# Kernel tuning notes

Hardware: AMD Instinct MI355X
Metric: run time of the kernel (lower is better)

## Reference

```python
import jax, jax.numpy as jnp
import numpy as np

DIM = 2048
NUM_HEADS = 16
HEAD_DIM = DIM // NUM_HEADS
ROPE_BASE = 10000.0


def _rope_cos_sin(seq_len, head_dim, dtype):
    # lucidrains-style interleaved rotary embedding
    inv_freq = 1.0 / (ROPE_BASE ** (jnp.arange(0, head_dim, 2, dtype=jnp.float32) / head_dim))
    t = jnp.arange(seq_len, dtype=jnp.float32)
    freqs = t[:, None] * inv_freq[None, :]            # [n, d/2]
    freqs = jnp.repeat(freqs, 2, axis=-1)             # [n, d] interleaved repeat
    return jnp.cos(freqs).astype(dtype), jnp.sin(freqs).astype(dtype)


def _rotate_half(x):
    # interleaved pairs: (x1, x2) -> (-x2, x1)
    x = x.reshape(x.shape[:-1] + (x.shape[-1] // 2, 2))
    x1, x2 = x[..., 0], x[..., 1]
    return jnp.stack((-x2, x1), axis=-1).reshape(x.shape[:-2] + (-1,))


def _apply_rope(x, cos, sin):
    # x: [b, h, n, d]; cos/sin: [n, d]
    return x * cos + _rotate_half(x) * sin


def setup_inputs() -> dict:
    key = jax.random.key(0)
    ks = jax.random.split(key, 9)
    s = 1.0 / np.sqrt(DIM)
    x = jax.random.normal(ks[0], (2, 2048, DIM), dtype=jnp.float32)
    Wq = jax.random.normal(ks[1], (DIM, DIM), dtype=jnp.float32) * s
    Wk = jax.random.normal(ks[2], (DIM, DIM), dtype=jnp.float32) * s
    Wv = jax.random.normal(ks[3], (DIM, DIM), dtype=jnp.float32) * s
    Wo = jax.random.normal(ks[4], (DIM, DIM), dtype=jnp.float32) * s
    bq = jax.random.normal(ks[5], (DIM,), dtype=jnp.float32) * 0.01
    bk = jax.random.normal(ks[6], (DIM,), dtype=jnp.float32) * 0.01
    bv = jax.random.normal(ks[7], (DIM,), dtype=jnp.float32) * 0.01
    bo = jax.random.normal(ks[8], (DIM,), dtype=jnp.float32) * 0.01
    return {"x": x, "Wq": Wq, "bq": bq, "Wk": Wk, "bk": bk,
            "Wv": Wv, "bv": bv, "Wo": Wo, "bo": bo}


def reference(x, Wq, bq, Wk, bk, Wv, bv, Wo, bo):
    b, n, _ = x.shape
    h, d = NUM_HEADS, HEAD_DIM
    # Q/K/V projections; weights stored as [in, out]
    q = (x @ Wq + bq).reshape(b, n, h, d).transpose(0, 2, 1, 3)  # [b,h,n,d]
    k = (x @ Wk + bk).reshape(b, n, h, d).transpose(0, 2, 1, 3)
    v = (x @ Wv + bv).reshape(b, n, h, d).transpose(0, 2, 1, 3)
    cos, sin = _rope_cos_sin(n, d, x.dtype)
    q = _apply_rope(q, cos, sin)
    k = _apply_rope(k, cos, sin)
    # module divides q by sqrt(d), then SDPA applies its own 1/sqrt(d)
    scale = 1.0 / jnp.sqrt(jnp.asarray(d, dtype=x.dtype))
    q = q * scale
    logits = jnp.einsum('bhqd,bhkd->bhqk', q, k) * scale
    attn = jax.nn.softmax(logits, axis=-1)
    out = jnp.einsum('bhqk,bhkd->bhqd', attn, v)          # [b,h,n,d]
    out = out.transpose(0, 2, 1, 3).reshape(b, n, h * d)  # [b,n,dim]
    return out @ Wo + bo
```

## Files before the change

kernel.cpp:

```cpp
#include <hip/hip_runtime.h>
#include <hip/hip_bf16.h>
#include <math.h>

typedef unsigned short u16;
typedef unsigned int u32;
typedef __attribute__((ext_vector_type(8))) short short8;
typedef __attribute__((ext_vector_type(4))) float f32x4;

typedef const __attribute__((address_space(1))) u32 gu32;
typedef __attribute__((address_space(3))) u32 lu32;

#define DIM 2048
#define SEQ 2048
#define BATCH 2
#define NH 16
#define HD 128
#define MTOT 4096

static __device__ __forceinline__ u16 f2b(float f) {
  __hip_bfloat16 h = __float2bfloat16(f);
  return __builtin_bit_cast(u16, h);
}
static __device__ __forceinline__ float b2f(u16 u) {
  __hip_bfloat16 h = __builtin_bit_cast(__hip_bfloat16, u);
  return __bfloat162float(h);
}

static __device__ __forceinline__ void g2l16(const u16* g, u16* l) {
  __builtin_amdgcn_global_load_lds((gu32*)g, (lu32*)l, 16, 0, 0);
}

__global__ __launch_bounds__(256) void conv_x_kernel(const float* __restrict__ x,
                                                     u16* __restrict__ xb) {
  size_t i = ((size_t)blockIdx.x * 256 + threadIdx.x) * 8;
  float4 a = *(const float4*)(x + i);
  float4 b = *(const float4*)(x + i + 4);
  uint4 o;
  o.x = (u32)f2b(a.x) | ((u32)f2b(a.y) << 16);
  o.y = (u32)f2b(a.z) | ((u32)f2b(a.w) << 16);
  o.z = (u32)f2b(b.x) | ((u32)f2b(b.y) << 16);
  o.w = (u32)f2b(b.z) | ((u32)f2b(b.w) << 16);
  *(uint4*)(xb + i) = o;
}

__global__ __launch_bounds__(256) void transw_kernel(const float* __restrict__ W0,
                                                     const float* __restrict__ W1,
                                                     const float* __restrict__ W2,
                                                     const float* __restrict__ W3,
                                                     u16* __restrict__ WT) {
  __shared__ float tile[64][65];
  const float* W = (blockIdx.z == 0) ? W0 : (blockIdx.z == 1) ? W1
                 : (blockIdx.z == 2) ? W2 : W3;
  u16* dst = WT + (size_t)blockIdx.z * DIM * DIM;
  int t = threadIdx.x;
  int k0 = blockIdx.y * 64, n0 = blockIdx.x * 64;
  int c = (t & 15) * 4;
  int r = t >> 4;
#pragma unroll
  for (int i = 0; i < 4; ++i) {
    float4 v = *(const float4*)(W + (size_t)(k0 + r + 16 * i) * DIM + n0 + c);
    tile[r + 16 * i][c + 0] = v.x;
    tile[r + 16 * i][c + 1] = v.y;
    tile[r + 16 * i][c + 2] = v.z;
    tile[r + 16 * i][c + 3] = v.w;
  }
  __syncthreads();
#pragma unroll
  for (int i = 0; i < 4; ++i) {
    int rn = r + 16 * i;
    uint2 o;
    o.x = (u32)f2b(tile[c + 0][rn]) | ((u32)f2b(tile[c + 1][rn]) << 16);
    o.y = (u32)f2b(tile[c + 2][rn]) | ((u32)f2b(tile[c + 3][rn]) << 16);
    *(uint2*)(dst + (size_t)(n0 + rn) * DIM + k0 + c) = o;
  }
}

__global__ __launch_bounds__(256) void rope_table_kernel(float* __restrict__ tab) {
  int idx = blockIdx.x * 256 + threadIdx.x;
  int n = idx >> 6, j = idx & 63;
  double ang = (double)n * pow(10000.0, -(double)j / 64.0);
  tab[2 * idx + 0] = (float)cos(ang);
  tab[2 * idx + 1] = (float)sin(ang);
}

__global__ __launch_bounds__(256) void rope_kernel(u16* __restrict__ Q,
                                                   u16* __restrict__ Kt,
                                                   const float* __restrict__ tab) {
  int idx = blockIdx.x * 256 + threadIdx.x;
  int which = idx >> 22;
  int rem = idx & ((1 << 22) - 1);
  int bh = rem >> 17;
  int r2 = rem & ((1 << 17) - 1);
  int n = r2 >> 6, j = r2 & 63;
  u16* p = (which ? Kt : Q) + ((size_t)bh * SEQ + n) * HD + 2 * j;
  float c = tab[2 * (n * 64 + j) + 0], s = tab[2 * (n * 64 + j) + 1];
  u32 v = *(const u32*)p;
  float x1 = b2f((u16)(v & 0xffff)), x2 = b2f((u16)(v >> 16));
  float sc = which ? 1.0f : (1.0f / 128.0f);
  float o1 = (x1 * c - x2 * s) * sc;
  float o2 = (x2 * c + x1 * s) * sc;
  *(u32*)p = (u32)f2b(o1) | ((u32)f2b(o2) << 16);
}

__global__ __launch_bounds__(256) void gemm_kernel(const u16* __restrict__ A,
                                                   const u16* __restrict__ Bt,
                                                   const float* __restrict__ bias,
                                                   void* __restrict__ Cout, int mode) {
  __shared__ u16 Asub[128 * 64];
  __shared__ u16 Bsub[128 * 64];
  int t = threadIdx.x;
  int lane = t & 63, wid = t >> 6;
  int L15 = lane & 15, quad = lane >> 4;
  int wm = (wid >> 1) * 64, wn = (wid & 1) * 64;
  int m0 = blockIdx.y * 128, n0 = blockIdx.x * 128;
  int srow = lane >> 3;
  int schunk = lane & 7;

  f32x4 acc[4][4];
#pragma unroll
  for (int mi = 0; mi < 4; ++mi)
#pragma unroll
    for (int ni = 0; ni < 4; ++ni)
#pragma unroll
      for (int r = 0; r < 4; ++r) acc[mi][ni][r] = 0.f;

  for (int k0 = 0; k0 < DIM; k0 += 64) {
#pragma unroll
    for (int i = 0; i < 4; ++i) {
      int ra = wid * 32 + i * 8 + srow;
      int cs = schunk ^ (ra & 7);
      g2l16(A + (size_t)(m0 + ra) * DIM + k0 + cs * 8,
            Asub + (size_t)(wid * 32 + i * 8) * 64);
      g2l16(Bt + (size_t)(n0 + ra) * DIM + k0 + cs * 8,
            Bsub + (size_t)(wid * 32 + i * 8) * 64);
    }
    __syncthreads();
#pragma unroll
    for (int kc = 0; kc < 2; ++kc) {
      short8 af[4], bfr[4];
#pragma unroll
      for (int mi = 0; mi < 4; ++mi) {
        int row = wm + mi * 16 + L15;
        af[mi] = *(const short8*)(Asub + row * 64 + (((kc * 4 + quad) ^ (L15 & 7)) * 8));
      }
#pragma unroll
      for (int ni = 0; ni < 4; ++ni) {
        int row = wn + ni * 16 + L15;
        bfr[ni] = *(const short8*)(Bsub + row * 64 + (((kc * 4 + quad) ^ (L15 & 7)) * 8));
      }
#pragma unroll
      for (int mi = 0; mi < 4; ++mi)
#pragma unroll
        for (int ni = 0; ni < 4; ++ni)
          acc[mi][ni] = __builtin_amdgcn_mfma_f32_16x16x32_bf16(af[mi], bfr[ni], acc[mi][ni], 0, 0, 0);
    }
    __syncthreads();
  }

#pragma unroll
  for (int mi = 0; mi < 4; ++mi) {
#pragma unroll
    for (int ni = 0; ni < 4; ++ni) {
      int col = n0 + wn + ni * 16 + L15;
      float bv = bias[col];
#pragma unroll
      for (int r = 0; r < 4; ++r) {
        int row = m0 + wm + mi * 16 + quad * 4 + r;
        float v = acc[mi][ni][r] + bv;
        if (mode == 2) {
          ((float*)Cout)[(size_t)row * DIM + col] = v;
        } else {
          int b = row >> 11, nseq = row & 2047;
          int h = col >> 7, d = col & 127;
          size_t idx;
          if (mode == 0)
            idx = ((size_t)(b * 16 + h) * SEQ + nseq) * HD + d;
          else
            idx = ((size_t)(b * 16 + h) * HD + d) * SEQ + nseq;
          ((u16*)Cout)[idx] = f2b(v);
        }
      }
    }
  }
}

__global__ __launch_bounds__(256, 4) void attn_kernel(const u16* __restrict__ Q,
                                                      const u16* __restrict__ K,
                                                      const u16* __restrict__ Vt,
                                                      u16* __restrict__ ctx) {
  __shared__ u16 Ksub[64 * 128];
  __shared__ u16 Vsub[128 * 64];
  __shared__ u16 Psub[4 * 16 * 64];
  int t = threadIdx.x;
  int lane = t & 63, wid = t >> 6;
  int L15 = lane & 15, quad = lane >> 4;
  int bh = blockIdx.y;
  int q0 = blockIdx.x * 64 + wid * 16;

  short8 qf[4];
  const u16* Qb = Q + ((size_t)bh * SEQ + q0) * HD;
#pragma unroll
  for (int kc = 0; kc < 4; ++kc)
    qf[kc] = *(const short8*)(Qb + (size_t)L15 * HD + kc * 32 + quad * 8);

  float lsum[4];
  f32x4 oacc[8];
#pragma unroll
  for (int r = 0; r < 4; ++r) lsum[r] = 0.f;
#pragma unroll
  for (int nt = 0; nt < 8; ++nt)
#pragma unroll
    for (int r = 0; r < 4; ++r) oacc[nt][r] = 0.f;

  const u16* Kb = K + (size_t)bh * SEQ * HD;
  const u16* Vb = Vt + (size_t)bh * HD * SEQ;
  u16* Pw = Psub + wid * 1024;

  int srowK = lane >> 4, schK = lane & 15;
  int srowV = lane >> 3, schV = lane & 7;

  for (int kt = 0; kt < SEQ; kt += 64) {
#pragma unroll
    for (int i = 0; i < 4; ++i) {
      int rk = wid * 16 + i * 4 + srowK;
      int ck = schK ^ (rk & 15);
      g2l16(Kb + (size_t)(kt + rk) * HD + ck * 8, Ksub + (size_t)(wid * 16 + i * 4) * 128);
      int rv = wid * 32 + i * 8 + srowV;
      int cv = schV ^ (rv & 7);
      g2l16(Vb + (size_t)rv * SEQ + kt + cv * 8, Vsub + (size_t)(wid * 32 + i * 8) * 64);
    }
    __syncthreads();

    f32x4 sacc[4];
#pragma unroll
    for (int nt = 0; nt < 4; ++nt)
#pragma unroll
      for (int r = 0; r < 4; ++r) sacc[nt][r] = 0.f;
#pragma unroll
    for (int nt = 0; nt < 4; ++nt)
#pragma unroll
      for (int kc = 0; kc < 4; ++kc) {
        int row = nt * 16 + L15;
        short8 kf = *(const short8*)(Ksub + row * 128 + (((kc * 4 + quad) ^ L15) * 8));
        sacc[nt] = __builtin_amdgcn_mfma_f32_16x16x32_bf16(qf[kc], kf, sacc[nt], 0, 0, 0);
      }

#pragma unroll
    for (int nt = 0; nt < 4; ++nt)
#pragma unroll
      for (int r = 0; r < 4; ++r) {
        float e = __expf(sacc[nt][r]);
        lsum[r] += e;
        int row = quad * 4 + r;
        int col = nt * 16 + L15;
        int ch = (col >> 3) ^ (row & 7);
        Pw[row * 64 + ch * 8 + (col & 7)] = f2b(e);
      }

#pragma unroll
    for (int kc = 0; kc < 2; ++kc) {
      short8 pf = *(const short8*)(Pw + L15 * 64 + (((kc * 4 + quad) ^ (L15 & 7)) * 8));
#pragma unroll
      for (int nt = 0; nt < 8; ++nt) {
        int row = nt * 16 + L15;
        short8 vf = *(const short8*)(Vsub + row * 64 + (((kc * 4 + quad) ^ (L15 & 7)) * 8));
        oacc[nt] = __builtin_amdgcn_mfma_f32_16x16x32_bf16(pf, vf, oacc[nt], 0, 0, 0);
      }
    }
    __syncthreads();
  }

#pragma unroll
  for (int off = 1; off < 16; off <<= 1)
#pragma unroll
    for (int r = 0; r < 4; ++r) lsum[r] += __shfl_xor(lsum[r], off, 64);

  int b = bh >> 4, h = bh & 15;
#pragma unroll
  for (int nt = 0; nt < 8; ++nt) {
    int d = nt * 16 + L15;
#pragma unroll
    for (int r = 0; r < 4; ++r) {
      int qrow = q0 + quad * 4 + r;
      float v = oacc[nt][r] / lsum[r];
      ctx[((size_t)b * SEQ + qrow) * DIM + h * HD + d] = f2b(v);
    }
  }
}

extern "C" void kernel_launch(void* const* d_in, const int* in_sizes, int n_in,
                              void* d_out, int out_size, void* d_ws, size_t ws_size,
                              hipStream_t stream) {
  (void)in_sizes; (void)n_in; (void)out_size; (void)ws_size;
  const float* x  = (const float*)d_in[0];
  const float* Wq = (const float*)d_in[1];
  const float* bq = (const float*)d_in[2];
  const float* Wk = (const float*)d_in[3];
  const float* bk = (const float*)d_in[4];
  const float* Wv = (const float*)d_in[5];
  const float* bv = (const float*)d_in[6];
  const float* Wo = (const float*)d_in[7];
  const float* bo = (const float*)d_in[8];

  u16* xb   = (u16*)d_ws;
  u16* WqT  = xb   + (size_t)8388608;
  u16* WkT  = WqT  + (size_t)4194304;
  u16* WvT  = WkT  + (size_t)4194304;
  u16* WoT  = WvT  + (size_t)4194304;
  u16* Qbuf = WoT  + (size_t)4194304;
  u16* Kbuf = Qbuf + (size_t)8388608;
  u16* Vtbf = Kbuf + (size_t)8388608;
  u16* ctx  = Vtbf + (size_t)8388608;
  float* tab = (float*)(ctx + (size_t)8388608);

  conv_x_kernel<<<4096, 256, 0, stream>>>(x, xb);
  transw_kernel<<<dim3(32, 32, 4), 256, 0, stream>>>(Wq, Wk, Wv, Wo, WqT);
  rope_table_kernel<<<512, 256, 0, stream>>>(tab);

  gemm_kernel<<<dim3(16, 32), 256, 0, stream>>>(xb, WqT, bq, Qbuf, 0);
  gemm_kernel<<<dim3(16, 32), 256, 0, stream>>>(xb, WkT, bk, Kbuf, 0);
  gemm_kernel<<<dim3(16, 32), 256, 0, stream>>>(xb, WvT, bv, Vtbf, 1);

  rope_kernel<<<32768, 256, 0, stream>>>(Qbuf, Kbuf, tab);

  attn_kernel<<<dim3(32, 32), 256, 0, stream>>>(Qbuf, Kbuf, Vtbf, ctx);

  gemm_kernel<<<dim3(16, 32), 256, 0, stream>>>(ctx, WoT, bo, d_out, 2);
}
```

Before: 451.6 us.

## Fuse prep kernels, merge QKV GEMMs with RoPE epilogue, double-buffer GEMM and attention

```diff
diff --git a/kernel.cpp b/kernel.cpp
--- a/kernel.cpp
+++ b/kernel.cpp
@@ -12,10 +12,8 @@
 
 #define DIM 2048
 #define SEQ 2048
-#define BATCH 2
 #define NH 16
 #define HD 128
-#define MTOT 4096
 
 static __device__ __forceinline__ u16 f2b(float f) {
   __hip_bfloat16 h = __float2bfloat16(f);
@@ -30,91 +28,80 @@
   __builtin_amdgcn_global_load_lds((gu32*)g, (lu32*)l, 16, 0, 0);
 }
 
-__global__ __launch_bounds__(256) void conv_x_kernel(const float* __restrict__ x,
-                                                     u16* __restrict__ xb) {
-  size_t i = ((size_t)blockIdx.x * 256 + threadIdx.x) * 8;
-  float4 a = *(const float4*)(x + i);
-  float4 b = *(const float4*)(x + i + 4);
-  uint4 o;
-  o.x = (u32)f2b(a.x) | ((u32)f2b(a.y) << 16);
-  o.y = (u32)f2b(a.z) | ((u32)f2b(a.w) << 16);
-  o.z = (u32)f2b(b.x) | ((u32)f2b(b.y) << 16);
-  o.w = (u32)f2b(b.z) | ((u32)f2b(b.w) << 16);
-  *(uint4*)(xb + i) = o;
-}
-
-__global__ __launch_bounds__(256) void transw_kernel(const float* __restrict__ W0,
-                                                     const float* __restrict__ W1,
-                                                     const float* __restrict__ W2,
-                                                     const float* __restrict__ W3,
-                                                     u16* __restrict__ WT) {
+__global__ __launch_bounds__(256) void prep_kernel(const float* __restrict__ x,
+                                                   const float* __restrict__ Wq,
+                                                   const float* __restrict__ Wk,
+                                                   const float* __restrict__ Wv,
+                                                   const float* __restrict__ Wo,
+                                                   u16* __restrict__ xb,
+                                                   u16* __restrict__ WT,
+                                                   float* __restrict__ tab) {
   __shared__ float tile[64][65];
-  const float* W = (blockIdx.z == 0) ? W0 : (blockIdx.z == 1) ? W1
-                 : (blockIdx.z == 2) ? W2 : W3;
-  u16* dst = WT + (size_t)blockIdx.z * DIM * DIM;
+  int bid = blockIdx.x;
   int t = threadIdx.x;
-  int k0 = blockIdx.y * 64, n0 = blockIdx.x * 64;
-  int c = (t & 15) * 4;
-  int r = t >> 4;
-#pragma unroll
-  for (int i = 0; i < 4; ++i) {
-    float4 v = *(const float4*)(W + (size_t)(k0 + r + 16 * i) * DIM + n0 + c);
-    tile[r + 16 * i][c + 0] = v.x;
-    tile[r + 16 * i][c + 1] = v.y;
-    tile[r + 16 * i][c + 2] = v.z;
-    tile[r + 16 * i][c + 3] = v.w;
-  }
-  __syncthreads();
-#pragma unroll
-  for (int i = 0; i < 4; ++i) {
-    int rn = r + 16 * i;
-    uint2 o;
-    o.x = (u32)f2b(tile[c + 0][rn]) | ((u32)f2b(tile[c + 1][rn]) << 16);
-    o.y = (u32)f2b(tile[c + 2][rn]) | ((u32)f2b(tile[c + 3][rn]) << 16);
-    *(uint2*)(dst + (size_t)(n0 + rn) * DIM + k0 + c) = o;
-  }
-}
-
-__global__ __launch_bounds__(256) void rope_table_kernel(float* __restrict__ tab) {
-  int idx = blockIdx.x * 256 + threadIdx.x;
-  int n = idx >> 6, j = idx & 63;
-  double ang = (double)n * pow(10000.0, -(double)j / 64.0);
-  tab[2 * idx + 0] = (float)cos(ang);
-  tab[2 * idx + 1] = (float)sin(ang);
-}
-
-__global__ __launch_bounds__(256) void rope_kernel(u16* __restrict__ Q,
-                                                   u16* __restrict__ Kt,
-                                                   const float* __restrict__ tab) {
-  int idx = blockIdx.x * 256 + threadIdx.x;
-  int which = idx >> 22;
-  int rem = idx & ((1 << 22) - 1);
-  int bh = rem >> 17;
-  int r2 = rem & ((1 << 17) - 1);
-  int n = r2 >> 6, j = r2 & 63;
-  u16* p = (which ? Kt : Q) + ((size_t)bh * SEQ + n) * HD + 2 * j;
-  float c = tab[2 * (n * 64 + j) + 0], s = tab[2 * (n * 64 + j) + 1];
-  u32 v = *(const u32*)p;
-  float x1 = b2f((u16)(v & 0xffff)), x2 = b2f((u16)(v >> 16));
-  float sc = which ? 1.0f : (1.0f / 128.0f);
-  float o1 = (x1 * c - x2 * s) * sc;
-  float o2 = (x2 * c + x1 * s) * sc;
-  *(u32*)p = (u32)f2b(o1) | ((u32)f2b(o2) << 16);
-}
-
-__global__ __launch_bounds__(256) void gemm_kernel(const u16* __restrict__ A,
-                                                   const u16* __restrict__ Bt,
-                                                   const float* __restrict__ bias,
-                                                   void* __restrict__ Cout, int mode) {
-  __shared__ u16 Asub[128 * 64];
-  __shared__ u16 Bsub[128 * 64];
+  if (bid < 4096) {
+    size_t i = ((size_t)bid * 256 + t) * 8;
+    float4 a = *(const float4*)(x + i);
+    float4 b = *(const float4*)(x + i + 4);
+    uint4 o;
+    o.x = (u32)f2b(a.x) | ((u32)f2b(a.y) << 16);
+    o.y = (u32)f2b(a.z) | ((u32)f2b(a.w) << 16);
+    o.z = (u32)f2b(b.x) | ((u32)f2b(b.y) << 16);
+    o.w = (u32)f2b(b.z) | ((u32)f2b(b.w) << 16);
+    *(uint4*)(xb + i) = o;
+  } else if (bid < 8192) {
+    int b2 = bid - 4096;
+    int z = b2 >> 10;
+    int rem = b2 & 1023;
+    int by = rem >> 5, bx = rem & 31;
+    const float* W = (z == 0) ? Wq : (z == 1) ? Wk : (z == 2) ? Wv : Wo;
+    u16* dst = WT + (size_t)z * DIM * DIM;
+    int k0 = by * 64, n0 = bx * 64;
+    int c = (t & 15) * 4;
+    int r = t >> 4;
+#pragma unroll
+    for (int i = 0; i < 4; ++i) {
+      float4 v = *(const float4*)(W + (size_t)(k0 + r + 16 * i) * DIM + n0 + c);
+      tile[r + 16 * i][c + 0] = v.x;
+      tile[r + 16 * i][c + 1] = v.y;
+      tile[r + 16 * i][c + 2] = v.z;
+      tile[r + 16 * i][c + 3] = v.w;
+    }
+    __syncthreads();
+#pragma unroll
+    for (int i = 0; i < 4; ++i) {
+      int rn = r + 16 * i;
+      uint2 o;
+      o.x = (u32)f2b(tile[c + 0][rn]) | ((u32)f2b(tile[c + 1][rn]) << 16);
+      o.y = (u32)f2b(tile[c + 2][rn]) | ((u32)f2b(tile[c + 3][rn]) << 16);
+      *(uint2*)(dst + (size_t)(n0 + rn) * DIM + k0 + c) = o;
+    }
+  } else {
+    int idx = (bid - 8192) * 256 + t;
+    int n = idx >> 6, j = idx & 63;
+    double ang = (double)n * pow(10000.0, -(double)j / 64.0);
+    tab[2 * idx + 0] = (float)cos(ang);
+    tab[2 * idx + 1] = (float)sin(ang);
+  }
+}
+
+__global__ __launch_bounds__(256, 2) void qkv_gemm_kernel(const u16* __restrict__ A,
+                                                          const u16* __restrict__ Bt,
+                                                          const float* __restrict__ bq,
+                                                          const float* __restrict__ bk,
+                                                          const float* __restrict__ bv,
+                                                          const float* __restrict__ tab,
+                                                          u16* __restrict__ Qbuf,
+                                                          u16* __restrict__ Kbuf,
+                                                          u16* __restrict__ Vtbf) {
+  __shared__ u16 Asub[2][128 * 64];
+  __shared__ u16 Bsub[2][128 * 64];
   int t = threadIdx.x;
   int lane = t & 63, wid = t >> 6;
   int L15 = lane & 15, quad = lane >> 4;
   int wm = (wid >> 1) * 64, wn = (wid & 1) * 64;
   int m0 = blockIdx.y * 128, n0 = blockIdx.x * 128;
-  int srow = lane >> 3;
-  int schunk = lane & 7;
+  int srow = lane >> 3, schunk = lane & 7;
 
   f32x4 acc[4][4];
 #pragma unroll
@@ -124,29 +111,33 @@
 #pragma unroll
       for (int r = 0; r < 4; ++r) acc[mi][ni][r] = 0.f;
 
-  for (int k0 = 0; k0 < DIM; k0 += 64) {
+  auto stage = [&](int buf, int k0) {
 #pragma unroll
     for (int i = 0; i < 4; ++i) {
       int ra = wid * 32 + i * 8 + srow;
       int cs = schunk ^ (ra & 7);
-      g2l16(A + (size_t)(m0 + ra) * DIM + k0 + cs * 8,
-            Asub + (size_t)(wid * 32 + i * 8) * 64);
-      g2l16(Bt + (size_t)(n0 + ra) * DIM + k0 + cs * 8,
-            Bsub + (size_t)(wid * 32 + i * 8) * 64);
-    }
+      g2l16(A + (size_t)(m0 + ra) * DIM + k0 + cs * 8, &Asub[buf][(wid * 32 + i * 8) * 64]);
+      g2l16(Bt + (size_t)(n0 + ra) * DIM + k0 + cs * 8, &Bsub[buf][(wid * 32 + i * 8) * 64]);
+    }
+  };
+
+  stage(0, 0);
+  for (int it = 0; it < DIM / 64; ++it) {
     __syncthreads();
+    if (it + 1 < DIM / 64) stage((it + 1) & 1, (it + 1) * 64);
+    int buf = it & 1;
 #pragma unroll
     for (int kc = 0; kc < 2; ++kc) {
       short8 af[4], bfr[4];
 #pragma unroll
       for (int mi = 0; mi < 4; ++mi) {
         int row = wm + mi * 16 + L15;
-        af[mi] = *(const short8*)(Asub + row * 64 + (((kc * 4 + quad) ^ (L15 & 7)) * 8));
+        af[mi] = *(const short8*)(&Asub[buf][row * 64 + (((kc * 4 + quad) ^ (L15 & 7)) * 8)]);
       }
 #pragma unroll
       for (int ni = 0; ni < 4; ++ni) {
         int row = wn + ni * 16 + L15;
-        bfr[ni] = *(const short8*)(Bsub + row * 64 + (((kc * 4 + quad) ^ (L15 & 7)) * 8));
+        bfr[ni] = *(const short8*)(&Bsub[buf][row * 64 + (((kc * 4 + quad) ^ (L15 & 7)) * 8)]);
       }
 #pragma unroll
       for (int mi = 0; mi < 4; ++mi)
@@ -154,7 +145,94 @@
         for (int ni = 0; ni < 4; ++ni)
           acc[mi][ni] = __builtin_amdgcn_mfma_f32_16x16x32_bf16(af[mi], bfr[ni], acc[mi][ni], 0, 0, 0);
     }
+  }
+
+  int which = n0 >> 11;
+  const float* bp = (which == 0) ? bq : (which == 1) ? bk : bv;
+#pragma unroll
+  for (int mi = 0; mi < 4; ++mi) {
+#pragma unroll
+    for (int ni = 0; ni < 4; ++ni) {
+      int colg = n0 + wn + ni * 16 + L15;
+      int col = colg & 2047;
+      float bvv = bp[col];
+      int h = col >> 7, d = col & 127;
+#pragma unroll
+      for (int r = 0; r < 4; ++r) {
+        int row = m0 + wm + mi * 16 + quad * 4 + r;
+        int b = row >> 11, nseq = row & 2047;
+        float v = acc[mi][ni][r] + bvv;
+        if (which < 2) {
+          int j = d >> 1;
+          float2 cs = ((const float2*)tab)[nseq * 64 + j];
+          float p = __shfl_xor(v, 1, 64);
+          float o = (d & 1) ? (v * cs.x + p * cs.y) : (v * cs.x - p * cs.y);
+          if (which == 0) o *= (1.0f / 128.0f);
+          u16* dst = (which == 0) ? Qbuf : Kbuf;
+          dst[((size_t)(b * 16 + h) * SEQ + nseq) * HD + d] = f2b(o);
+        } else {
+          Vtbf[((size_t)(b * 16 + h) * HD + d) * SEQ + nseq] = f2b(v);
+        }
+      }
+    }
+  }
+}
+
+__global__ __launch_bounds__(256, 2) void o_gemm_kernel(const u16* __restrict__ A,
+                                                        const u16* __restrict__ Bt,
+                                                        const float* __restrict__ bias,
+                                                        float* __restrict__ Cout) {
+  __shared__ u16 Asub[2][128 * 64];
+  __shared__ u16 Bsub[2][128 * 64];
+  int t = threadIdx.x;
+  int lane = t & 63, wid = t >> 6;
+  int L15 = lane & 15, quad = lane >> 4;
+  int wm = (wid >> 1) * 64, wn = (wid & 1) * 64;
+  int m0 = blockIdx.y * 128, n0 = blockIdx.x * 128;
+  int srow = lane >> 3, schunk = lane & 7;
+
+  f32x4 acc[4][4];
+#pragma unroll
+  for (int mi = 0; mi < 4; ++mi)
+#pragma unroll
+    for (int ni = 0; ni < 4; ++ni)
+#pragma unroll
+      for (int r = 0; r < 4; ++r) acc[mi][ni][r] = 0.f;
+
+  auto stage = [&](int buf, int k0) {
+#pragma unroll
+    for (int i = 0; i < 4; ++i) {
+      int ra = wid * 32 + i * 8 + srow;
+      int cs = schunk ^ (ra & 7);
+      g2l16(A + (size_t)(m0 + ra) * DIM + k0 + cs * 8, &Asub[buf][(wid * 32 + i * 8) * 64]);
+      g2l16(Bt + (size_t)(n0 + ra) * DIM + k0 + cs * 8, &Bsub[buf][(wid * 32 + i * 8) * 64]);
+    }
+  };
+
+  stage(0, 0);
+  for (int it = 0; it < DIM / 64; ++it) {
     __syncthreads();
+    if (it + 1 < DIM / 64) stage((it + 1) & 1, (it + 1) * 64);
+    int buf = it & 1;
+#pragma unroll
+    for (int kc = 0; kc < 2; ++kc) {
+      short8 af[4], bfr[4];
+#pragma unroll
+      for (int mi = 0; mi < 4; ++mi) {
+        int row = wm + mi * 16 + L15;
+        af[mi] = *(const short8*)(&Asub[buf][row * 64 + (((kc * 4 + quad) ^ (L15 & 7)) * 8)]);
+      }
+#pragma unroll
+      for (int ni = 0; ni < 4; ++ni) {
+        int row = wn + ni * 16 + L15;
+        bfr[ni] = *(const short8*)(&Bsub[buf][row * 64 + (((kc * 4 + quad) ^ (L15 & 7)) * 8)]);
+      }
+#pragma unroll
+      for (int mi = 0; mi < 4; ++mi)
+#pragma unroll
+        for (int ni = 0; ni < 4; ++ni)
+          acc[mi][ni] = __builtin_amdgcn_mfma_f32_16x16x32_bf16(af[mi], bfr[ni], acc[mi][ni], 0, 0, 0);
+    }
   }
 
 #pragma unroll
@@ -162,40 +240,28 @@
 #pragma unroll
     for (int ni = 0; ni < 4; ++ni) {
       int col = n0 + wn + ni * 16 + L15;
-      float bv = bias[col];
+      float bvv = bias[col];
 #pragma unroll
       for (int r = 0; r < 4; ++r) {
         int row = m0 + wm + mi * 16 + quad * 4 + r;
-        float v = acc[mi][ni][r] + bv;
-        if (mode == 2) {
-          ((float*)Cout)[(size_t)row * DIM + col] = v;
-        } else {
-          int b = row >> 11, nseq = row & 2047;
-          int h = col >> 7, d = col & 127;
-          size_t idx;
-          if (mode == 0)
-            idx = ((size_t)(b * 16 + h) * SEQ + nseq) * HD + d;
-          else
-            idx = ((size_t)(b * 16 + h) * HD + d) * SEQ + nseq;
-          ((u16*)Cout)[idx] = f2b(v);
-        }
-      }
-    }
-  }
-}
-
-__global__ __launch_bounds__(256, 4) void attn_kernel(const u16* __restrict__ Q,
+        Cout[(size_t)row * DIM + col] = acc[mi][ni][r] + bvv;
+      }
+    }
+  }
+}
+
+__global__ __launch_bounds__(512, 4) void attn_kernel(const u16* __restrict__ Q,
                                                       const u16* __restrict__ K,
                                                       const u16* __restrict__ Vt,
                                                       u16* __restrict__ ctx) {
-  __shared__ u16 Ksub[64 * 128];
-  __shared__ u16 Vsub[128 * 64];
-  __shared__ u16 Psub[4 * 16 * 64];
+  __shared__ u16 Ksub[2][64 * 128];
+  __shared__ u16 Vsub[2][128 * 64];
+  __shared__ u16 Psub[8][16 * 64];
   int t = threadIdx.x;
   int lane = t & 63, wid = t >> 6;
   int L15 = lane & 15, quad = lane >> 4;
   int bh = blockIdx.y;
-  int q0 = blockIdx.x * 64 + wid * 16;
+  int q0 = blockIdx.x * 128 + wid * 16;
 
   short8 qf[4];
   const u16* Qb = Q + ((size_t)bh * SEQ + q0) * HD;
@@ -214,22 +280,29 @@
 
   const u16* Kb = K + (size_t)bh * SEQ * HD;
   const u16* Vb = Vt + (size_t)bh * HD * SEQ;
-  u16* Pw = Psub + wid * 1024;
-
-  int srowK = lane >> 4, schK = lane & 15;
-  int srowV = lane >> 3, schV = lane & 7;
-
-  for (int kt = 0; kt < SEQ; kt += 64) {
-#pragma unroll
-    for (int i = 0; i < 4; ++i) {
-      int rk = wid * 16 + i * 4 + srowK;
-      int ck = schK ^ (rk & 15);
-      g2l16(Kb + (size_t)(kt + rk) * HD + ck * 8, Ksub + (size_t)(wid * 16 + i * 4) * 128);
-      int rv = wid * 32 + i * 8 + srowV;
-      int cv = schV ^ (rv & 7);
-      g2l16(Vb + (size_t)rv * SEQ + kt + cv * 8, Vsub + (size_t)(wid * 32 + i * 8) * 64);
-    }
+  u16* Pw = &Psub[wid][0];
+
+  int rkl = lane >> 4, ckl = lane & 15;
+  int rvl = lane >> 3, cvl = lane & 7;
+
+  auto stage = [&](int buf, int kt) {
+#pragma unroll
+    for (int i = 0; i < 2; ++i) {
+      int j = wid + i * 8;
+      int rk = j * 4 + rkl;
+      int ck = ckl ^ (rk & 15);
+      g2l16(Kb + (size_t)(kt + rk) * HD + ck * 8, &Ksub[buf][j * 4 * 128]);
+      int rv = j * 8 + rvl;
+      int cv = cvl ^ (rv & 7);
+      g2l16(Vb + (size_t)rv * SEQ + kt + cv * 8, &Vsub[buf][j * 8 * 64]);
+    }
+  };
+
+  stage(0, 0);
+  for (int it = 0; it < SEQ / 64; ++it) {
     __syncthreads();
+    if (it + 1 < SEQ / 64) stage((it + 1) & 1, (it + 1) * 64);
+    int buf = it & 1;
 
     f32x4 sacc[4];
 #pragma unroll
@@ -241,7 +314,7 @@
 #pragma unroll
       for (int kc = 0; kc < 4; ++kc) {
         int row = nt * 16 + L15;
-        short8 kf = *(const short8*)(Ksub + row * 128 + (((kc * 4 + quad) ^ L15) * 8));
+        short8 kf = *(const short8*)(&Ksub[buf][row * 128 + (((kc * 4 + quad) ^ L15) * 8)]);
         sacc[nt] = __builtin_amdgcn_mfma_f32_16x16x32_bf16(qf[kc], kf, sacc[nt], 0, 0, 0);
       }
 
@@ -263,11 +336,10 @@
 #pragma unroll
       for (int nt = 0; nt < 8; ++nt) {
         int row = nt * 16 + L15;
-        short8 vf = *(const short8*)(Vsub + row * 64 + (((kc * 4 + quad) ^ (L15 & 7)) * 8));
+        short8 vf = *(const short8*)(&Vsub[buf][row * 64 + (((kc * 4 + quad) ^ (L15 & 7)) * 8)]);
         oacc[nt] = __builtin_amdgcn_mfma_f32_16x16x32_bf16(pf, vf, oacc[nt], 0, 0, 0);
       }
     }
-    __syncthreads();
   }
 
 #pragma unroll
@@ -303,27 +375,17 @@
   const float* bo = (const float*)d_in[8];
 
   u16* xb   = (u16*)d_ws;
-  u16* WqT  = xb   + (size_t)8388608;
-  u16* WkT  = WqT  + (size_t)4194304;
-  u16* WvT  = WkT  + (size_t)4194304;
-  u16* WoT  = WvT  + (size_t)4194304;
-  u16* Qbuf = WoT  + (size_t)4194304;
+  u16* WT   = xb   + (size_t)8388608;
+  u16* Qbuf = WT   + (size_t)4 * 4194304;
   u16* Kbuf = Qbuf + (size_t)8388608;
   u16* Vtbf = Kbuf + (size_t)8388608;
   u16* ctx  = Vtbf + (size_t)8388608;
   float* tab = (float*)(ctx + (size_t)8388608);
 
-  conv_x_kernel<<<4096, 256, 0, stream>>>(x, xb);
-  transw_kernel<<<dim3(32, 32, 4), 256, 0, stream>>>(Wq, Wk, Wv, Wo, WqT);
-  rope_table_kernel<<<512, 256, 0, stream>>>(tab);
-
-  gemm_kernel<<<dim3(16, 32), 256, 0, stream>>>(xb, WqT, bq, Qbuf, 0);
-  gemm_kernel<<<dim3(16, 32), 256, 0, stream>>>(xb, WkT, bk, Kbuf, 0);
-  gemm_kernel<<<dim3(16, 32), 256, 0, stream>>>(xb, WvT, bv, Vtbf, 1);
-
-  rope_kernel<<<32768, 256, 0, stream>>>(Qbuf, Kbuf, tab);
-
-  attn_kernel<<<dim3(32, 32), 256, 0, stream>>>(Qbuf, Kbuf, Vtbf, ctx);
-
-  gemm_kernel<<<dim3(16, 32), 256, 0, stream>>>(ctx, WoT, bo, d_out, 2);
-}
+  prep_kernel<<<8704, 256, 0, stream>>>(x, Wq, Wk, Wv, Wo, xb, WT, tab);
+  qkv_gemm_kernel<<<dim3(48, 32), 256, 0, stream>>>(xb, WT, bq, bk, bv, tab,
+                                                    Qbuf, Kbuf, Vtbf);
+  attn_kernel<<<dim3(16, 32), 512, 0, stream>>>(Qbuf, Kbuf, Vtbf, ctx);
+  o_gemm_kernel<<<dim3(16, 32), 256, 0, stream>>>(ctx, WT + (size_t)3 * 4194304, bo,
+                                                  (float*)d_out);
+}
```

New measurement: 434.3 us. 3.8% less time.
